# Kernel tuning notes

Measured on AMD Instinct MI355X. Metric: run time of the kernel, lower is better.

Reference implementation:

```python
import jax, jax.numpy as jnp
import numpy as np

CH = 128          # channels
R1 = 8            # ch_reduction1 -> theta/phi dim = 16
R2 = 2            # ch_reduction2 -> g dim = 64
D = 2             # downsampling (maxpool kernel/stride on w,h)


def _conv1x1x1(x, w, b):
    # x: (b, cin, n, w, h); w: (cout, cin); b: (cout,)
    return jnp.einsum('bcnwh,oc->bonwh', x, w) + b[None, :, None, None, None]


def _maxpool_wh(x):
    # 2x2 max pool (stride 2) over the last two dims; x: (b, c, n, w, h)
    b, c, n, w, h = x.shape
    return x.reshape(b, c, n, w // D, D, h // D, D).max(axis=(4, 6))


def setup_inputs() -> dict:
    key = jax.random.key(0)
    ks = jax.random.split(key, 9)
    c1, c2 = CH // R1, CH // R2
    s = lambda fan: 1.0 / np.sqrt(fan)
    return {
        'x': jax.random.normal(ks[0], (2, CH, 16, 32, 32), jnp.float32),
        'w_theta': jax.random.normal(ks[1], (c1, CH), jnp.float32) * s(CH),
        'b_theta': jnp.zeros((c1,), jnp.float32),
        'w_phi': jax.random.normal(ks[2], (c1, CH), jnp.float32) * s(CH),
        'b_phi': jnp.zeros((c1,), jnp.float32),
        'w_g': jax.random.normal(ks[3], (c2, CH), jnp.float32) * s(CH),
        'b_g': jnp.zeros((c2,), jnp.float32),
        'w_attn_g': jax.random.normal(ks[4], (CH, c2), jnp.float32) * s(c2),
        'b_attn_g': jnp.zeros((CH,), jnp.float32),
        'gamma': jnp.zeros((1,), jnp.float32),  # initial_gamma = 0
    }


def reference(x, w_theta, b_theta, w_phi, b_phi, w_g, b_g, w_attn_g, b_attn_g, gamma):
    bs, ch, n, w, h = x.shape
    N = n * w * h                       # query locations
    M = n * (w // D) * (h // D)         # pooled key/value locations

    # theta: (bs, N, c1)
    theta = jnp.tanh(_conv1x1x1(x, w_theta, b_theta))
    theta = theta.transpose(0, 2, 3, 4, 1).reshape(bs, N, -1)

    # phi: tanh proj -> maxpool over w,h -> (bs, M, c1)
    phi = _maxpool_wh(jnp.tanh(_conv1x1x1(x, w_phi, b_phi)))
    phi = phi.transpose(0, 2, 3, 4, 1).reshape(bs, M, -1)

    # dot-product kernel; softmax over dim=1 (QUERY axis), as in the torch code
    attn = jax.nn.softmax(jnp.einsum('bnc,bmc->bnm', theta, phi), axis=1)

    # g: proj -> maxpool -> (bs, M, c2)
    g = _maxpool_wh(_conv1x1x1(x, w_g, b_g))
    g = g.transpose(0, 2, 3, 4, 1).reshape(bs, M, -1)

    # attend and fold back to (bs, c2, n, w, h)
    attn_g = jnp.einsum('bnm,bmc->bnc', attn, g)
    attn_g = attn_g.reshape(bs, n, w, h, -1).transpose(0, 4, 1, 2, 3)
    attn_g = _conv1x1x1(attn_g, w_attn_g, b_attn_g)

    alpha = jax.nn.sigmoid(gamma)[0]
    out = (1.0 - alpha) * x + alpha * attn_g
    return (out, attn_g)
```

## Files before the change

kernel.cpp:

```cpp
#include <hip/hip_runtime.h>

typedef short bf16x8 __attribute__((ext_vector_type(8)));
typedef float f32x16 __attribute__((ext_vector_type(16)));

#define DI __device__ __forceinline__

constexpr int BS = 2, CH = 128;
constexpr int NQ = 16384, NM = 4096;
constexpr size_t NX = (size_t)BS * CH * NQ;

DI float bf2f(ushort u) { unsigned v = ((unsigned)u) << 16; return __builtin_bit_cast(float, v); }
DI ushort f2bf(float f) {
  unsigned u = __builtin_bit_cast(unsigned, f);
  u += 0x7FFFu + ((u >> 16) & 1u);
  return (ushort)(u >> 16);
}
DI float ldany(const void* p, size_t i, int f) {
  return f ? ((const float*)p)[i] : bf2f(((const ushort*)p)[i]);
}
DI f32x16 mfma_bf16(bf16x8 a, bf16x8 b, f32x16 c) {
  return __builtin_amdgcn_mfma_f32_32x32x16_bf16(a, b, c, 0, 0, 0);
}
DI float fexp2(float x) { return __builtin_amdgcn_exp2f(x); }

__global__ void k_sniff(const void* __restrict__ x, int* __restrict__ flag) {
  if (threadIdx.x == 0 && blockIdx.x == 0) {
    const ushort* u = (const ushort*)x;
    int garbage = 0, zeros = 0;
    for (int i = 0; i < 256; ++i) {
      float v = bf2f(u[i]);
      if (!(fabsf(v) < 1e9f)) garbage++;
      if ((i & 1) == 0 && u[i] == 0) zeros++;
    }
    flag[0] = (garbage >= 8 || zeros >= 100) ? 1 : 0;
  }
}

__global__ __launch_bounds__(256) void k_prep(
    const void* __restrict__ wT, const void* __restrict__ bT,
    const void* __restrict__ wP, const void* __restrict__ bP,
    const void* __restrict__ wG, const void* __restrict__ bG,
    const void* __restrict__ wAG, const void* __restrict__ bAG,
    const int* __restrict__ flag,
    float* __restrict__ bAllf, uint4* __restrict__ wF, uint4* __restrict__ wBf)
{
  int t = threadIdx.x;
  int f = flag[0];
  if (blockIdx.x == 0) {
    if (t < 16)  bAllf[t]       = ldany(bT, t, f);
    if (t < 16)  bAllf[16 + t]  = ldany(bP, t, f);
    if (t < 64)  bAllf[32 + t]  = ldany(bG, t, f);
    if (t < 128) bAllf[96 + t]  = ldany(bAG, t, f);
  } else if (blockIdx.x <= 4) {
    int idx = (blockIdx.x - 1) * 256 + t;
    int lane = idx & 63, ks = (idx >> 6) & 3, ot = idx >> 8;
    size_t src = (size_t)(ot * 32 + (lane & 31)) * 64 + ks * 16 + (lane >> 5) * 8;
    union { uint4 v4; ushort s[8]; } o;
    #pragma unroll
    for (int j = 0; j < 8; ++j) o.s[j] = f2bf(ldany(wAG, src + j, f));
    wF[idx] = o.v4;
  } else {
    int idx = (int)(blockIdx.x - 5) * 256 + t;
    int kb = idx / 192, rem = idx % 192;
    int ob = rem >> 6, lane = rem & 63;
    int r = ob * 32 + (lane & 31);
    int c = kb * 16 + (lane >> 5) * 8;
    const void* src; int row;
    if (r < 16)      { src = wT; row = r; }
    else if (r < 32) { src = wP; row = r - 16; }
    else             { src = wG; row = r - 32; }
    union { uint4 v4; ushort s[8]; } o;
    #pragma unroll
    for (int j = 0; j < 8; ++j) o.s[j] = f2bf(ldany(src, (size_t)row * 128 + c + j, f));
    wBf[(kb * 3 + ob) * 64 + lane] = o.v4;
  }
}

__global__ __launch_bounds__(128) void k_proj(
    const void* __restrict__ x, const int* __restrict__ flag,
    const uint4* __restrict__ wBf, const float* __restrict__ bAllf,
    ushort* __restrict__ theta, ushort* __restrict__ phi, ushort* __restrict__ gm)
{
  int b = blockIdx.y;
  int qt = blockIdx.x;
  int t = threadIdx.x;
  int w = t >> 6, l = t & 63, lr = l & 31, lh = l >> 5;
  int f = flag[0];

  __shared__ float tile[64][33];

  size_t xbase = (size_t)b * CH * NQ + qt * 64 + w * 32 + lr;

  f32x16 acc0, acc1, acc2;
  #pragma unroll
  for (int i = 0; i < 16; ++i) { acc0[i] = 0.f; acc1[i] = 0.f; acc2[i] = 0.f; }

  #pragma unroll
  for (int kb = 0; kb < 8; ++kb) {
    union { uint4 v4; ushort s[8]; } a;
    int cb = kb * 16 + lh * 8;
    if (f) {
      const float* xf = (const float*)x;
      #pragma unroll
      for (int j = 0; j < 8; ++j) a.s[j] = f2bf(xf[xbase + (size_t)(cb + j) * NQ]);
    } else {
      const ushort* xu = (const ushort*)x;
      #pragma unroll
      for (int j = 0; j < 8; ++j) a.s[j] = xu[xbase + (size_t)(cb + j) * NQ];
    }
    bf16x8 aF = __builtin_bit_cast(bf16x8, a.v4);
    uint4 b0 = wBf[(kb * 3 + 0) * 64 + l];
    uint4 b1 = wBf[(kb * 3 + 1) * 64 + l];
    uint4 b2 = wBf[(kb * 3 + 2) * 64 + l];
    acc0 = mfma_bf16(aF, __builtin_bit_cast(bf16x8, b0), acc0);
    acc1 = mfma_bf16(aF, __builtin_bit_cast(bf16x8, b1), acc1);
    acc2 = mfma_bf16(aF, __builtin_bit_cast(bf16x8, b2), acc2);
  }

  constexpr float L2E = 1.4426950408889634f;

  #pragma unroll
  for (int ob = 0; ob < 3; ++ob) {
    __syncthreads();
    {
      f32x16 A = (ob == 0) ? acc0 : ((ob == 1) ? acc1 : acc2);
      #pragma unroll
      for (int r = 0; r < 16; ++r) {
        int qq = (r & 3) + 8 * (r >> 2) + 4 * lh;
        tile[w * 32 + qq][lr] = A[r];
      }
    }
    __syncthreads();
    if (ob == 0) {
      if (t < 64) {
        union { uint4 v4[2]; ushort s[16]; } th;
        #pragma unroll
        for (int c = 0; c < 16; ++c)
          th.s[c] = f2bf(tanhf(tile[t][c] + bAllf[c]) * L2E);
        uint4* dst = (uint4*)(theta + ((size_t)b * NQ + qt * 64 + t) * 16);
        dst[0] = th.v4[0]; dst[1] = th.v4[1];
      } else {
        int idx = t - 64;
        int m = idx >> 2, c4 = (idx & 3) * 4;
        int h2 = m * 2;
        union { uint2 v2; ushort s[4]; } ph;
        #pragma unroll
        for (int cc = 0; cc < 4; ++cc) {
          int c = 16 + c4 + cc;
          float z = fmaxf(fmaxf(tile[h2][c], tile[h2 + 1][c]),
                          fmaxf(tile[32 + h2][c], tile[32 + h2 + 1][c]));
          ph.s[cc] = f2bf(tanhf(z + bAllf[c]));
        }
        *(uint2*)(phi + ((size_t)b * NM + qt * 16 + m) * 16 + c4) = ph.v2;
      }
    } else {
      int cb = (ob - 1) * 32;
      int m = t >> 3, c4 = (t & 7) * 4;
      int h2 = m * 2;
      union { uint2 v2; ushort s[4]; } gv;
      #pragma unroll
      for (int cc = 0; cc < 4; ++cc) {
        int c = c4 + cc;
        float z = fmaxf(fmaxf(tile[h2][c], tile[h2 + 1][c]),
                        fmaxf(tile[32 + h2][c], tile[32 + h2 + 1][c]));
        gv.s[cc] = f2bf(z + bAllf[32 + cb + c]);
      }
      *(uint2*)(gm + ((size_t)b * NM + qt * 16 + m) * 64 + cb + c4) = gv.v2;
    }
  }
}

__global__ __launch_bounds__(256, 6) void k_denom(
    const ushort* __restrict__ theta, const ushort* __restrict__ phi,
    float* __restrict__ partial)
{
  int b = blockIdx.z, qs = blockIdx.y;
  int w = threadIdx.x >> 6;
  int l = threadIdx.x & 63, lr = l & 31, lh = l >> 5;
  int m0 = blockIdx.x * 128 + w * 32;

  bf16x8 pB = __builtin_bit_cast(bf16x8, *(const uint4*)(phi + ((size_t)b * NM + m0 + lr) * 16 + lh * 8));
  const ushort* thb = theta + ((size_t)b * NQ + qs * 512 + lr) * 16 + lh * 8;

  bf16x8 tA1 = __builtin_bit_cast(bf16x8, *(const uint4*)(thb + 512));
  f32x16 S;
  #pragma unroll
  for (int i = 0; i < 16; ++i) S[i] = 0.f;
  S = mfma_bf16(__builtin_bit_cast(bf16x8, *(const uint4*)thb), pB, S);

  float s = 0.f;
  for (int it = 0; it < 16; ++it) {
    bf16x8 tA2 = __builtin_bit_cast(bf16x8, *(const uint4*)(thb + (size_t)((it + 2) & 15) * 512));
    __builtin_amdgcn_sched_barrier(0);
    f32x16 Sn;
    #pragma unroll
    for (int i = 0; i < 16; ++i) Sn[i] = 0.f;
    Sn = mfma_bf16(tA1, pB, Sn);
    #pragma unroll
    for (int r = 0; r < 16; ++r) s += fexp2(S[r]);
    S = Sn; tA1 = tA2;
  }
  s += __shfl_xor(s, 32, 64);
  if (l < 32) partial[(((size_t)b * 32 + qs) << 12) + m0 + lr] = s;
}

__global__ __launch_bounds__(256) void k_gsf(
    const float* __restrict__ partial, const ushort* __restrict__ gm,
    uint4* __restrict__ gsF)
{
  int b = blockIdx.y, mb = blockIdx.x;
  int t = threadIdx.x;
  int mbase = mb * 32;

  __shared__ float dinv_sh[32];
  __shared__ float tile[32][65];

  if (t < 32) {
    int m = mbase + t;
    float s = 0.f;
    #pragma unroll
    for (int p = 0; p < 32; ++p) s += partial[(((size_t)b * 32 + p) << 12) + m];
    dinv_sh[t] = 1.f / s;
  }
  __syncthreads();

  {
    int m_loc = t >> 3, c = (t & 7) * 8;
    union { uint4 v4; ushort s[8]; } v;
    v.v4 = *(const uint4*)(gm + ((size_t)b * NM + mbase + m_loc) * 64 + c);
    float dv = dinv_sh[m_loc];
    #pragma unroll
    for (int j = 0; j < 8; ++j) tile[m_loc][c + j] = bf2f(v.s[j]) * dv;
  }
  __syncthreads();

  int ms_loc = t >> 7, ct = (t >> 6) & 1, lane = t & 63;
  int col = ct * 32 + (lane & 31);
  int rbase = ms_loc * 16 + (lane >> 5) * 8;
  union { uint4 v4; ushort s[8]; } o;
  #pragma unroll
  for (int j = 0; j < 8; ++j) o.s[j] = f2bf(tile[rbase + j][col]);
  int ms = (mbase >> 4) + ms_loc;
  gsF[(((size_t)b * 256 + ms) * 2 + ct) * 64 + lane] = o.v4;
}

__global__ __launch_bounds__(256, 3) void k_attn(
    const ushort* __restrict__ theta, const ushort* __restrict__ phi,
    const uint4* __restrict__ gsF, const uint4* __restrict__ wF,
    const float* __restrict__ bAllf, const void* __restrict__ x,
    const void* __restrict__ gamma, const int* __restrict__ flag,
    void* __restrict__ out_base)
{
  int b = blockIdx.y;
  int q0 = blockIdx.x * 64;
  int t = threadIdx.x;
  int mq = t >> 6, l = t & 63, lr = l & 31, lh = l >> 5;

  __shared__ float agPart[4][32][65];
  __shared__ __align__(16) ushort agF[32][80];

  bf16x8 tB0 = __builtin_bit_cast(bf16x8, *(const uint4*)(theta + ((size_t)b * NQ + q0 + lr) * 16 + lh * 8));
  bf16x8 tB1 = __builtin_bit_cast(bf16x8, *(const uint4*)(theta + ((size_t)b * NQ + q0 + 32 + lr) * 16 + lh * 8));

  const ushort* phb = phi + ((size_t)b * NM + lr) * 16 + lh * 8;
  const uint4* gF = gsF + (size_t)b * 32768;

  f32x16 a00, a01, a10, a11;
  #pragma unroll
  for (int i = 0; i < 16; ++i) { a00[i] = 0.f; a01[i] = 0.f; a10[i] = 0.f; a11[i] = 0.f; }
  f32x16 zero16;
  #pragma unroll
  for (int i = 0; i < 16; ++i) zero16[i] = 0.f;

  size_t gb0 = (size_t)(mq * 2) * 128;
  uint4 g00 = gF[gb0 + l];
  uint4 g01 = gF[gb0 + 64 + l];
  uint4 g10 = gF[gb0 + 128 + l];
  uint4 g11 = gF[gb0 + 192 + l];
  bf16x8 pA = __builtin_bit_cast(bf16x8, *(const uint4*)(phb + (size_t)(mq * 32) * 16));

  for (int it = 0; it < 32; ++it) {
    int it1 = (it + 1) & 31;
    size_t gb = (size_t)(mq * 2 + it1 * 8) * 128;
    uint4 n00 = gF[gb + l];
    uint4 n01 = gF[gb + 64 + l];
    uint4 n10 = gF[gb + 128 + l];
    uint4 n11 = gF[gb + 192 + l];
    bf16x8 pAn = __builtin_bit_cast(bf16x8, *(const uint4*)(phb + (size_t)(mq * 32 + it1 * 128) * 16));
    __builtin_amdgcn_sched_barrier(0);

    f32x16 Sa = mfma_bf16(pA, tB0, zero16);
    f32x16 Sb = mfma_bf16(pA, tB1, zero16);

    uint u0, u1, u2, u3, u4, u5, u6, u7;

    #pragma unroll
    for (int r = 0; r < 16; ++r) Sa[r] = fexp2(Sa[r]);
    asm("v_cvt_pk_bf16_f32 %0, %1, %2" : "=v"(u0) : "v"(Sa[0]),  "v"(Sa[1]));
    asm("v_cvt_pk_bf16_f32 %0, %1, %2" : "=v"(u1) : "v"(Sa[2]),  "v"(Sa[3]));
    asm("v_cvt_pk_bf16_f32 %0, %1, %2" : "=v"(u2) : "v"(Sa[4]),  "v"(Sa[5]));
    asm("v_cvt_pk_bf16_f32 %0, %1, %2" : "=v"(u3) : "v"(Sa[6]),  "v"(Sa[7]));
    asm("v_cvt_pk_bf16_f32 %0, %1, %2" : "=v"(u4) : "v"(Sa[8]),  "v"(Sa[9]));
    asm("v_cvt_pk_bf16_f32 %0, %1, %2" : "=v"(u5) : "v"(Sa[10]), "v"(Sa[11]));
    asm("v_cvt_pk_bf16_f32 %0, %1, %2" : "=v"(u6) : "v"(Sa[12]), "v"(Sa[13]));
    asm("v_cvt_pk_bf16_f32 %0, %1, %2" : "=v"(u7) : "v"(Sa[14]), "v"(Sa[15]));
    asm("v_permlane32_swap_b32 %0, %1" : "+v"(u0), "+v"(u2));
    asm("v_permlane32_swap_b32 %0, %1" : "+v"(u1), "+v"(u3));
    asm("v_permlane32_swap_b32 %0, %1" : "+v"(u4), "+v"(u6));
    asm("v_permlane32_swap_b32 %0, %1" : "+v"(u5), "+v"(u7));
    {
      uint4 fa0 = make_uint4(u0, u1, u2, u3);
      uint4 fa1 = make_uint4(u4, u5, u6, u7);
      a00 = mfma_bf16(__builtin_bit_cast(bf16x8, fa0), __builtin_bit_cast(bf16x8, g00), a00);
      a01 = mfma_bf16(__builtin_bit_cast(bf16x8, fa0), __builtin_bit_cast(bf16x8, g01), a01);
      a00 = mfma_bf16(__builtin_bit_cast(bf16x8, fa1), __builtin_bit_cast(bf16x8, g10), a00);
      a01 = mfma_bf16(__builtin_bit_cast(bf16x8, fa1), __builtin_bit_cast(bf16x8, g11), a01);
    }

    #pragma unroll
    for (int r = 0; r < 16; ++r) Sb[r] = fexp2(Sb[r]);
    asm("v_cvt_pk_bf16_f32 %0, %1, %2" : "=v"(u0) : "v"(Sb[0]),  "v"(Sb[1]));
    asm("v_cvt_pk_bf16_f32 %0, %1, %2" : "=v"(u1) : "v"(Sb[2]),  "v"(Sb[3]));
    asm("v_cvt_pk_bf16_f32 %0, %1, %2" : "=v"(u2) : "v"(Sb[4]),  "v"(Sb[5]));
    asm("v_cvt_pk_bf16_f32 %0, %1, %2" : "=v"(u3) : "v"(Sb[6]),  "v"(Sb[7]));
    asm("v_cvt_pk_bf16_f32 %0, %1, %2" : "=v"(u4) : "v"(Sb[8]),  "v"(Sb[9]));
    asm("v_cvt_pk_bf16_f32 %0, %1, %2" : "=v"(u5) : "v"(Sb[10]), "v"(Sb[11]));
    asm("v_cvt_pk_bf16_f32 %0, %1, %2" : "=v"(u6) : "v"(Sb[12]), "v"(Sb[13]));
    asm("v_cvt_pk_bf16_f32 %0, %1, %2" : "=v"(u7) : "v"(Sb[14]), "v"(Sb[15]));
    asm("v_permlane32_swap_b32 %0, %1" : "+v"(u0), "+v"(u2));
    asm("v_permlane32_swap_b32 %0, %1" : "+v"(u1), "+v"(u3));
    asm("v_permlane32_swap_b32 %0, %1" : "+v"(u4), "+v"(u6));
    asm("v_permlane32_swap_b32 %0, %1" : "+v"(u5), "+v"(u7));
    {
      uint4 fb0 = make_uint4(u0, u1, u2, u3);
      uint4 fb1 = make_uint4(u4, u5, u6, u7);
      a10 = mfma_bf16(__builtin_bit_cast(bf16x8, fb0), __builtin_bit_cast(bf16x8, g00), a10);
      a11 = mfma_bf16(__builtin_bit_cast(bf16x8, fb0), __builtin_bit_cast(bf16x8, g01), a11);
      a10 = mfma_bf16(__builtin_bit_cast(bf16x8, fb1), __builtin_bit_cast(bf16x8, g10), a10);
      a11 = mfma_bf16(__builtin_bit_cast(bf16x8, fb1), __builtin_bit_cast(bf16x8, g11), a11);
    }

    pA = pAn;
    g00 = n00; g01 = n01; g10 = n10; g11 = n11;
  }

  int mode = flag[0];
  float ga = ldany(gamma, 0, mode);
  float alpha = 1.f / (1.f + __expf(-ga));

  #pragma unroll
  for (int h = 0; h < 2; ++h) {
    __syncthreads();
    {
      f32x16 ac0 = (h == 0) ? a00 : a10;
      f32x16 ac1 = (h == 0) ? a01 : a11;
      #pragma unroll
      for (int r = 0; r < 16; ++r) {
        int qq = (r & 3) + 8 * (r >> 2) + 4 * lh;
        agPart[mq][qq][lr]      = ac0[r];
        agPart[mq][qq][32 + lr] = ac1[r];
      }
    }
    __syncthreads();
    {
      #pragma unroll
      for (int jj = 0; jj < 8; ++jj) {
        int c = mq * 16 + lh * 8 + jj;
        float vsum = agPart[0][lr][c] + agPart[1][lr][c] + agPart[2][lr][c] + agPart[3][lr][c];
        agF[lr][c] = f2bf(vsum);
      }
    }
    __syncthreads();
    {
      f32x16 oacc;
      #pragma unroll
      for (int i = 0; i < 16; ++i) oacc[i] = 0.f;
      #pragma unroll
      for (int ks = 0; ks < 4; ++ks) {
        bf16x8 aw = __builtin_bit_cast(bf16x8, wF[(mq * 4 + ks) * 64 + l]);
        bf16x8 bg = __builtin_bit_cast(bf16x8, *(const uint4*)&agF[lr][ks * 16 + lh * 8]);
        oacc = mfma_bf16(aw, bg, oacc);
      }
      if (mode) {
        float* o0 = (float*)out_base;
        float* o1 = o0 + NX;
        const float* xf = (const float*)x;
        #pragma unroll
        for (int r = 0; r < 16; ++r) {
          int o = mq * 32 + (r & 3) + 8 * (r >> 2) + 4 * lh;
          size_t oi = ((size_t)b * CH + o) * NQ + q0 + h * 32 + lr;
          float ag = oacc[r] + bAllf[96 + o];
          o0[oi] = (1.f - alpha) * xf[oi] + alpha * ag;
          o1[oi] = ag;
        }
      } else {
        ushort* o0 = (ushort*)out_base;
        ushort* o1 = o0 + NX;
        const ushort* xu = (const ushort*)x;
        #pragma unroll
        for (int r = 0; r < 16; ++r) {
          int o = mq * 32 + (r & 3) + 8 * (r >> 2) + 4 * lh;
          size_t oi = ((size_t)b * CH + o) * NQ + q0 + h * 32 + lr;
          float ag = oacc[r] + bAllf[96 + o];
          o0[oi] = f2bf((1.f - alpha) * bf2f(xu[oi]) + alpha * ag);
          o1[oi] = f2bf(ag);
        }
      }
    }
  }
}

extern "C" void kernel_launch(void* const* d_in, const int* in_sizes, int n_in,
                              void* d_out, int out_size, void* d_ws, size_t ws_size,
                              hipStream_t stream) {
  const void* x    = d_in[0];
  const void* wT   = d_in[1];
  const void* bT   = d_in[2];
  const void* wP   = d_in[3];
  const void* bP   = d_in[4];
  const void* wG   = d_in[5];
  const void* bG   = d_in[6];
  const void* wAG  = d_in[7];
  const void* bAG  = d_in[8];
  const void* gmm  = d_in[9];

  char* ws = (char*)d_ws;
  ushort* theta  = (ushort*)(ws + 0);
  ushort* phi    = (ushort*)(ws + 1048576);
  ushort* gm     = (ushort*)(ws + 1310720);
  float*  part   = (float*) (ws + 2359296);
  uint4*  gsF    = (uint4*) (ws + 3407872);
  uint4*  wF     = (uint4*) (ws + 4456448);
  uint4*  wBf    = (uint4*) (ws + 4472832);
  float*  bAllf  = (float*) (ws + 4497408);
  int*    flag   = (int*)   (ws + 4498432);

  k_sniff<<<dim3(1), dim3(64), 0, stream>>>(x, flag);
  k_prep<<<dim3(11), dim3(256), 0, stream>>>(wT, bT, wP, bP, wG, bG, wAG, bAG, flag, bAllf, wF, wBf);
  k_proj<<<dim3(256, 2), dim3(128), 0, stream>>>(x, flag, wBf, bAllf, theta, phi, gm);
  k_denom<<<dim3(32, 32, 2), dim3(256), 0, stream>>>(theta, phi, part);
  k_gsf<<<dim3(128, 2), dim3(256), 0, stream>>>(part, gm, gsF);
  k_attn<<<dim3(256, 2), dim3(256), 0, stream>>>(theta, phi, gsF, wF, bAllf, x, gmm, flag, d_out);
}
```

Measured before the change: 78.97 us.

## Fuse sniff into prep, split-K projection, merge denominator and g-scaling kernels

Folds the input-format sniff into each prep block, removing one kernel launch. The projection kernel now uses 256 threads, with two waves splitting the channel reduction and summing their results through shared memory. The softmax denominator and g-scaling kernels are merged into one 1024-thread block per 32 keys. That block reduces the column sums across all queries in shared memory, so the partial buffer in global memory and one more launch go away. The cost is fewer blocks (256) in the denominator stage, each with a longer serial loop, plus extra barriers in the projection kernel.

```diff
diff --git a/kernel.cpp b/kernel.cpp
--- a/kernel.cpp
+++ b/kernel.cpp
@@ -23,29 +23,36 @@
 }
 DI float fexp2(float x) { return __builtin_amdgcn_exp2f(x); }
 
-__global__ void k_sniff(const void* __restrict__ x, int* __restrict__ flag) {
-  if (threadIdx.x == 0 && blockIdx.x == 0) {
-    const ushort* u = (const ushort*)x;
-    int garbage = 0, zeros = 0;
-    for (int i = 0; i < 256; ++i) {
-      float v = bf2f(u[i]);
-      if (!(fabsf(v) < 1e9f)) garbage++;
-      if ((i & 1) == 0 && u[i] == 0) zeros++;
-    }
-    flag[0] = (garbage >= 8 || zeros >= 100) ? 1 : 0;
-  }
+DI int sniff_local(const void* x) {
+  const ushort* u = (const ushort*)x;
+  int garbage = 0, zeros = 0;
+  for (int i = 0; i < 256; ++i) {
+    float v = bf2f(u[i]);
+    if (!(fabsf(v) < 1e9f)) garbage++;
+    if ((i & 1) == 0 && u[i] == 0) zeros++;
+  }
+  return (garbage >= 8 || zeros >= 100) ? 1 : 0;
 }
 
 __global__ __launch_bounds__(256) void k_prep(
+    const void* __restrict__ x,
     const void* __restrict__ wT, const void* __restrict__ bT,
     const void* __restrict__ wP, const void* __restrict__ bP,
     const void* __restrict__ wG, const void* __restrict__ bG,
     const void* __restrict__ wAG, const void* __restrict__ bAG,
-    const int* __restrict__ flag,
+    int* __restrict__ flag,
     float* __restrict__ bAllf, uint4* __restrict__ wF, uint4* __restrict__ wBf)
 {
   int t = threadIdx.x;
-  int f = flag[0];
+  __shared__ int fsh;
+  if (t == 0) {
+    int f = sniff_local(x);
+    fsh = f;
+    if (blockIdx.x == 0) flag[0] = f;
+  }
+  __syncthreads();
+  int f = fsh;
+
   if (blockIdx.x == 0) {
     if (t < 16)  bAllf[t]       = ldany(bT, t, f);
     if (t < 16)  bAllf[16 + t]  = ldany(bP, t, f);
@@ -76,7 +83,7 @@
   }
 }
 
-__global__ __launch_bounds__(128) void k_proj(
+__global__ __launch_bounds__(256) void k_proj(
     const void* __restrict__ x, const int* __restrict__ flag,
     const uint4* __restrict__ wBf, const float* __restrict__ bAllf,
     ushort* __restrict__ theta, ushort* __restrict__ phi, ushort* __restrict__ gm)
@@ -85,18 +92,20 @@
   int qt = blockIdx.x;
   int t = threadIdx.x;
   int w = t >> 6, l = t & 63, lr = l & 31, lh = l >> 5;
+  int qhalf = w & 1, khalf = w >> 1;
   int f = flag[0];
 
   __shared__ float tile[64][33];
 
-  size_t xbase = (size_t)b * CH * NQ + qt * 64 + w * 32 + lr;
+  size_t xbase = (size_t)b * CH * NQ + qt * 64 + qhalf * 32 + lr;
 
   f32x16 acc0, acc1, acc2;
   #pragma unroll
   for (int i = 0; i < 16; ++i) { acc0[i] = 0.f; acc1[i] = 0.f; acc2[i] = 0.f; }
 
   #pragma unroll
-  for (int kb = 0; kb < 8; ++kb) {
+  for (int kk = 0; kk < 4; ++kk) {
+    int kb = khalf * 4 + kk;
     union { uint4 v4; ushort s[8]; } a;
     int cb = kb * 16 + lh * 8;
     if (f) {
@@ -121,13 +130,21 @@
 
   #pragma unroll
   for (int ob = 0; ob < 3; ++ob) {
-    __syncthreads();
-    {
-      f32x16 A = (ob == 0) ? acc0 : ((ob == 1) ? acc1 : acc2);
+    f32x16 A = (ob == 0) ? acc0 : ((ob == 1) ? acc1 : acc2);
+    __syncthreads();
+    if (khalf == 1) {
       #pragma unroll
       for (int r = 0; r < 16; ++r) {
         int qq = (r & 3) + 8 * (r >> 2) + 4 * lh;
-        tile[w * 32 + qq][lr] = A[r];
+        tile[qhalf * 32 + qq][lr] = A[r];
+      }
+    }
+    __syncthreads();
+    if (khalf == 0) {
+      #pragma unroll
+      for (int r = 0; r < 16; ++r) {
+        int qq = (r & 3) + 8 * (r >> 2) + 4 * lh;
+        tile[qhalf * 32 + qq][lr] += A[r];
       }
     }
     __syncthreads();
@@ -139,7 +156,7 @@
           th.s[c] = f2bf(tanhf(tile[t][c] + bAllf[c]) * L2E);
         uint4* dst = (uint4*)(theta + ((size_t)b * NQ + qt * 64 + t) * 16);
         dst[0] = th.v4[0]; dst[1] = th.v4[1];
-      } else {
+      } else if (t < 128) {
         int idx = t - 64;
         int m = idx >> 2, c4 = (idx & 3) * 4;
         int h2 = m * 2;
@@ -154,77 +171,71 @@
         *(uint2*)(phi + ((size_t)b * NM + qt * 16 + m) * 16 + c4) = ph.v2;
       }
     } else {
-      int cb = (ob - 1) * 32;
-      int m = t >> 3, c4 = (t & 7) * 4;
-      int h2 = m * 2;
-      union { uint2 v2; ushort s[4]; } gv;
-      #pragma unroll
-      for (int cc = 0; cc < 4; ++cc) {
-        int c = c4 + cc;
-        float z = fmaxf(fmaxf(tile[h2][c], tile[h2 + 1][c]),
-                        fmaxf(tile[32 + h2][c], tile[32 + h2 + 1][c]));
-        gv.s[cc] = f2bf(z + bAllf[32 + cb + c]);
-      }
-      *(uint2*)(gm + ((size_t)b * NM + qt * 16 + m) * 64 + cb + c4) = gv.v2;
-    }
-  }
-}
-
-__global__ __launch_bounds__(256, 6) void k_denom(
+      if (t < 128) {
+        int cb = (ob - 1) * 32;
+        int m = t >> 3, c4 = (t & 7) * 4;
+        int h2 = m * 2;
+        union { uint2 v2; ushort s[4]; } gv;
+        #pragma unroll
+        for (int cc = 0; cc < 4; ++cc) {
+          int c = c4 + cc;
+          float z = fmaxf(fmaxf(tile[h2][c], tile[h2 + 1][c]),
+                          fmaxf(tile[32 + h2][c], tile[32 + h2 + 1][c]));
+          gv.s[cc] = f2bf(z + bAllf[32 + cb + c]);
+        }
+        *(uint2*)(gm + ((size_t)b * NM + qt * 16 + m) * 64 + cb + c4) = gv.v2;
+      }
+    }
+  }
+}
+
+__global__ __launch_bounds__(1024, 2) void k_denom2(
     const ushort* __restrict__ theta, const ushort* __restrict__ phi,
-    float* __restrict__ partial)
-{
-  int b = blockIdx.z, qs = blockIdx.y;
-  int w = threadIdx.x >> 6;
-  int l = threadIdx.x & 63, lr = l & 31, lh = l >> 5;
-  int m0 = blockIdx.x * 128 + w * 32;
-
-  bf16x8 pB = __builtin_bit_cast(bf16x8, *(const uint4*)(phi + ((size_t)b * NM + m0 + lr) * 16 + lh * 8));
-  const ushort* thb = theta + ((size_t)b * NQ + qs * 512 + lr) * 16 + lh * 8;
-
-  bf16x8 tA1 = __builtin_bit_cast(bf16x8, *(const uint4*)(thb + 512));
-  f32x16 S;
-  #pragma unroll
-  for (int i = 0; i < 16; ++i) S[i] = 0.f;
-  S = mfma_bf16(__builtin_bit_cast(bf16x8, *(const uint4*)thb), pB, S);
-
-  float s = 0.f;
-  for (int it = 0; it < 16; ++it) {
-    bf16x8 tA2 = __builtin_bit_cast(bf16x8, *(const uint4*)(thb + (size_t)((it + 2) & 15) * 512));
-    __builtin_amdgcn_sched_barrier(0);
-    f32x16 Sn;
-    #pragma unroll
-    for (int i = 0; i < 16; ++i) Sn[i] = 0.f;
-    Sn = mfma_bf16(tA1, pB, Sn);
-    #pragma unroll
-    for (int r = 0; r < 16; ++r) s += fexp2(S[r]);
-    S = Sn; tA1 = tA2;
-  }
-  s += __shfl_xor(s, 32, 64);
-  if (l < 32) partial[(((size_t)b * 32 + qs) << 12) + m0 + lr] = s;
-}
-
-__global__ __launch_bounds__(256) void k_gsf(
-    const float* __restrict__ partial, const ushort* __restrict__ gm,
-    uint4* __restrict__ gsF)
+    const ushort* __restrict__ gm, uint4* __restrict__ gsF)
 {
   int b = blockIdx.y, mb = blockIdx.x;
   int t = threadIdx.x;
+  int w = t >> 6, l = t & 63, lr = l & 31, lh = l >> 5;
   int mbase = mb * 32;
 
+  __shared__ float part[16][33];
   __shared__ float dinv_sh[32];
   __shared__ float tile[32][65];
 
+  bf16x8 pB = __builtin_bit_cast(bf16x8, *(const uint4*)(phi + ((size_t)b * NM + mbase + lr) * 16 + lh * 8));
+  const ushort* thb = theta + ((size_t)b * NQ + w * 1024 + lr) * 16 + lh * 8;
+
+  bf16x8 tA1 = __builtin_bit_cast(bf16x8, *(const uint4*)(thb + 512));
+  f32x16 S;
+  #pragma unroll
+  for (int i = 0; i < 16; ++i) S[i] = 0.f;
+  S = mfma_bf16(__builtin_bit_cast(bf16x8, *(const uint4*)thb), pB, S);
+
+  float s = 0.f;
+  for (int it = 0; it < 32; ++it) {
+    bf16x8 tA2 = __builtin_bit_cast(bf16x8, *(const uint4*)(thb + (size_t)((it + 2) & 31) * 512));
+    __builtin_amdgcn_sched_barrier(0);
+    f32x16 Sn;
+    #pragma unroll
+    for (int i = 0; i < 16; ++i) Sn[i] = 0.f;
+    Sn = mfma_bf16(tA1, pB, Sn);
+    #pragma unroll
+    for (int r = 0; r < 16; ++r) s += fexp2(S[r]);
+    S = Sn; tA1 = tA2;
+  }
+  s += __shfl_xor(s, 32, 64);
+  if (l < 32) part[w][lr] = s;
+  __syncthreads();
+
   if (t < 32) {
-    int m = mbase + t;
-    float s = 0.f;
-    #pragma unroll
-    for (int p = 0; p < 32; ++p) s += partial[(((size_t)b * 32 + p) << 12) + m];
-    dinv_sh[t] = 1.f / s;
+    float d = 0.f;
+    #pragma unroll
+    for (int p = 0; p < 16; ++p) d += part[p][t];
+    dinv_sh[t] = 1.f / d;
   }
   __syncthreads();
 
-  {
+  if (t < 256) {
     int m_loc = t >> 3, c = (t & 7) * 8;
     union { uint4 v4; ushort s[8]; } v;
     v.v4 = *(const uint4*)(gm + ((size_t)b * NM + mbase + m_loc) * 64 + c);
@@ -234,14 +245,16 @@
   }
   __syncthreads();
 
-  int ms_loc = t >> 7, ct = (t >> 6) & 1, lane = t & 63;
-  int col = ct * 32 + (lane & 31);
-  int rbase = ms_loc * 16 + (lane >> 5) * 8;
-  union { uint4 v4; ushort s[8]; } o;
-  #pragma unroll
-  for (int j = 0; j < 8; ++j) o.s[j] = f2bf(tile[rbase + j][col]);
-  int ms = (mbase >> 4) + ms_loc;
-  gsF[(((size_t)b * 256 + ms) * 2 + ct) * 64 + lane] = o.v4;
+  if (t < 256) {
+    int ms_loc = t >> 7, ct = (t >> 6) & 1, lane = t & 63;
+    int col = ct * 32 + (lane & 31);
+    int rbase = ms_loc * 16 + (lane >> 5) * 8;
+    union { uint4 v4; ushort s[8]; } o;
+    #pragma unroll
+    for (int j = 0; j < 8; ++j) o.s[j] = f2bf(tile[rbase + j][col]);
+    int ms = (mbase >> 4) + ms_loc;
+    gsF[(((size_t)b * 256 + ms) * 2 + ct) * 64 + lane] = o.v4;
+  }
 }
 
 __global__ __launch_bounds__(256, 3) void k_attn(
@@ -428,17 +441,14 @@
   ushort* theta  = (ushort*)(ws + 0);
   ushort* phi    = (ushort*)(ws + 1048576);
   ushort* gm     = (ushort*)(ws + 1310720);
-  float*  part   = (float*) (ws + 2359296);
   uint4*  gsF    = (uint4*) (ws + 3407872);
   uint4*  wF     = (uint4*) (ws + 4456448);
   uint4*  wBf    = (uint4*) (ws + 4472832);
   float*  bAllf  = (float*) (ws + 4497408);
   int*    flag   = (int*)   (ws + 4498432);
 
-  k_sniff<<<dim3(1), dim3(64), 0, stream>>>(x, flag);
-  k_prep<<<dim3(11), dim3(256), 0, stream>>>(wT, bT, wP, bP, wG, bG, wAG, bAG, flag, bAllf, wF, wBf);
-  k_proj<<<dim3(256, 2), dim3(128), 0, stream>>>(x, flag, wBf, bAllf, theta, phi, gm);
-  k_denom<<<dim3(32, 32, 2), dim3(256), 0, stream>>>(theta, phi, part);
-  k_gsf<<<dim3(128, 2), dim3(256), 0, stream>>>(part, gm, gsF);
+  k_prep<<<dim3(11), dim3(256), 0, stream>>>(x, wT, bT, wP, bP, wG, bG, wAG, bAG, flag, bAllf, wF, wBf);
+  k_proj<<<dim3(256, 2), dim3(256), 0, stream>>>(x, flag, wBf, bAllf, theta, phi, gm);
+  k_denom2<<<dim3(128, 2), dim3(1024), 0, stream>>>(theta, phi, gm, gsF);
   k_attn<<<dim3(256, 2), dim3(256), 0, stream>>>(theta, phi, gsF, wF, bAllf, x, gmm, flag, d_out);
 }
```

Measured after the change: 73.21 us (median of 3 runs). 7.3% less time.
